# Optimization experiments

Measured on AMD Instinct MI355X. Metric: run time of the kernel, lower is better.

## Reference

```python
import jax, jax.numpy as jnp
import numpy as np

TEM = 0.5
BN_EPS = 1e-5
ROWS, IN_FEA, OUT_FEA = 16384, 512, 128


def setup_inputs() -> dict:
    key = jax.random.key(0)
    ks = jax.random.split(key, 3)
    doc_fea = jax.random.normal(ks[0], (ROWS, IN_FEA), dtype=jnp.float32)
    W1 = jax.random.normal(ks[1], (IN_FEA, OUT_FEA), dtype=jnp.float32) * 0.02
    b1 = jnp.zeros((OUT_FEA,), dtype=jnp.float32)
    gamma = jnp.ones((OUT_FEA,), dtype=jnp.float32)
    beta = jnp.zeros((OUT_FEA,), dtype=jnp.float32)
    W2 = jax.random.normal(ks[2], (OUT_FEA, OUT_FEA), dtype=jnp.float32) * 0.02
    b2 = jnp.zeros((OUT_FEA,), dtype=jnp.float32)
    return {"doc_fea": doc_fea, "W1": W1, "b1": b1, "gamma": gamma,
            "beta": beta, "W2": W2, "b2": b2}


def _l2_normalize(x):
    # matches torch F.normalize(dim=1, eps=1e-12)
    n = jnp.linalg.norm(x, axis=1, keepdims=True)
    return x / jnp.maximum(n, 1e-12)


def _half_loss(a, b):
    # rows of a, b are unit-norm, so cosine sim == matmul
    between = jnp.exp(a @ b.T / TEM)          # [N, N]
    refl = jnp.exp(a @ a.T / TEM)             # [N, N]
    pos = jnp.diagonal(between)
    denom = refl.sum(axis=1) + between.sum(axis=1) - jnp.diagonal(refl)
    return -jnp.log(pos / denom)


def reference(doc_fea, W1, b1, gamma, beta, W2, b2):
    # projector: Linear -> BatchNorm1d (training stats) -> ReLU -> Linear
    h = doc_fea @ W1 + b1
    mu = h.mean(axis=0)
    var = h.var(axis=0)  # biased variance, as used by torch BN normalization
    h = (h - mu) * jax.lax.rsqrt(var + BN_EPS) * gamma + beta
    h = jax.nn.relu(h)
    out = h @ W2 + b2
    out = _l2_normalize(out)
    # original: out_1 = out[indices where i%2!=0], out_2 = out[i%2==0]
    out_1 = out[1::2]
    out_2 = out[0::2]
    l1 = _half_loss(out_1, out_2)
    l2 = _half_loss(out_2, out_1)
    loss = (l1 + l2) * 0.5
    return loss.mean()
```

## Files before the change

kernel.cpp:

```cpp
#include <hip/hip_runtime.h>

typedef __attribute__((ext_vector_type(8))) short short8;
typedef __attribute__((ext_vector_type(4))) float f32x4;

typedef const __attribute__((address_space(1))) unsigned int as1_u32;
typedef __attribute__((address_space(3))) unsigned int as3_u32;

#define E2f   7.38905609893065f
#define OSCALE 1.69864357f

#define EXP2(x) exp2f(x)

__device__ inline unsigned short f2bf(float f){
    union { float f; unsigned int u; } x; x.f = f;
    unsigned int u = x.u;
    return (unsigned short)((u + 0x7fffu + ((u >> 16) & 1u)) >> 16);
}

__device__ inline short8 pack8(float4 a, float4 b){
    short8 t;
    t[0]=(short)f2bf(a.x); t[1]=(short)f2bf(a.y); t[2]=(short)f2bf(a.z); t[3]=(short)f2bf(a.w);
    t[4]=(short)f2bf(b.x); t[5]=(short)f2bf(b.y); t[6]=(short)f2bf(b.z); t[7]=(short)f2bf(b.w);
    return t;
}

__global__ __launch_bounds__(256) void k_prep(const float* __restrict__ W1, const float* __restrict__ W2,
                                              short* __restrict__ W1T, short* __restrict__ W2T){
    int idx = blockIdx.x*256 + threadIdx.x;
    if(idx < 512*128){
        int n = idx >> 9, k = idx & 511;
        W1T[idx] = (short)f2bf(W1[k*128 + n]);
    } else {
        int i2 = idx - 512*128;
        int n = i2 >> 7, k = i2 & 127;
        W2T[i2] = (short)f2bf(W2[k*128 + n]);
    }
}

__global__ __launch_bounds__(256) void k_gemm1(const float* __restrict__ doc, const float* __restrict__ b1,
                                               const short* __restrict__ W1T, float* __restrict__ h,
                                               float* __restrict__ bsum, float* __restrict__ bsq){
    int bid = blockIdx.x;
    int tid = threadIdx.x;
    int w = tid >> 6, l = tid & 63, lr = l & 15, lk = l >> 4;
    int rowA = bid*64 + w*16 + lr;

    short8 a[16];
    const float* dp = doc + rowA*512 + lk*8;
    #pragma unroll
    for(int c=0;c<16;c++){
        float4 f0 = *(const float4*)(dp + c*32);
        float4 f1 = *(const float4*)(dp + c*32 + 4);
        a[c] = pack8(f0, f1);
    }

    f32x4 acc[8];
    #pragma unroll
    for(int ct=0; ct<8; ct++) acc[ct] = (f32x4){0.f,0.f,0.f,0.f};

    const short* wb = W1T + lr*512 + lk*8;
    #pragma unroll
    for(int c=0;c<16;c++){
        #pragma unroll
        for(int ct=0; ct<8; ct++){
            short8 b = *(const short8*)(wb + ct*16*512 + c*32);
            acc[ct] = __builtin_amdgcn_mfma_f32_16x16x32_bf16(a[c], b, acc[ct], 0,0,0);
        }
    }

    __shared__ float lds_s[4][128];
    __shared__ float lds_q[4][128];
    int rowD = bid*64 + w*16 + lk*4;
    #pragma unroll
    for(int ct=0; ct<8; ct++){
        float bb = b1[ct*16 + lr];
        float s = 0.f, q = 0.f;
        #pragma unroll
        for(int r=0;r<4;r++){
            float v = acc[ct][r] + bb;
            h[(rowD + r)*128 + ct*16 + lr] = v;
            s += v; q += v*v;
        }
        s += __shfl_xor(s,16); s += __shfl_xor(s,32);
        q += __shfl_xor(q,16); q += __shfl_xor(q,32);
        if(lk==0){ lds_s[w][ct*16+lr] = s; lds_q[w][ct*16+lr] = q; }
    }
    __syncthreads();
    if(tid < 128){
        float S = lds_s[0][tid]+lds_s[1][tid]+lds_s[2][tid]+lds_s[3][tid];
        float Q = lds_q[0][tid]+lds_q[1][tid]+lds_q[2][tid]+lds_q[3][tid];
        bsum[bid*128 + tid] = S;
        bsq [bid*128 + tid] = Q;
    }
}

__global__ __launch_bounds__(1024) void k_bnfin(const float* __restrict__ bsum, const float* __restrict__ bsq,
                                                const float* __restrict__ gamma, const float* __restrict__ beta,
                                                float* __restrict__ bnA, float* __restrict__ bnB){
    int tid = threadIdx.x;
    int c = tid & 127, seg = tid >> 7;
    float S=0.f, Q=0.f;
    for(int b=seg*32; b<seg*32+32; b++){ S += bsum[b*128+c]; Q += bsq[b*128+c]; }
    __shared__ float ls[8][128], lq[8][128];
    ls[seg][c] = S; lq[seg][c] = Q;
    __syncthreads();
    if(tid < 128){
        float St=0.f, Qt=0.f;
        #pragma unroll
        for(int s=0;s<8;s++){ St += ls[s][tid]; Qt += lq[s][tid]; }
        float mu = St * (1.0f/16384.0f);
        float var = Qt * (1.0f/16384.0f) - mu*mu;
        float A = gamma[tid] * rsqrtf(var + 1e-5f);
        bnA[tid] = A;
        bnB[tid] = beta[tid] - mu*A;
    }
}

__global__ __launch_bounds__(256) void k_gemm2(const float* __restrict__ h, const short* __restrict__ W2T,
                                               const float* __restrict__ bnA, const float* __restrict__ bnB,
                                               const float* __restrict__ b2,
                                               short* __restrict__ o1s, short* __restrict__ o2s,
                                               float* __restrict__ dvec){
    int bid = blockIdx.x;
    int tid = threadIdx.x;
    int w = tid >> 6, l = tid & 63, lr = l & 15, lk = l >> 4;
    int rowA = bid*64 + w*16 + lr;

    short8 a[4];
    const float* hp = h + rowA*128 + lk*8;
    #pragma unroll
    for(int c=0;c<4;c++){
        float4 h0 = *(const float4*)(hp + c*32);
        float4 h1 = *(const float4*)(hp + c*32 + 4);
        float4 A0 = *(const float4*)(bnA + c*32 + lk*8);
        float4 A1 = *(const float4*)(bnA + c*32 + lk*8 + 4);
        float4 B0 = *(const float4*)(bnB + c*32 + lk*8);
        float4 B1 = *(const float4*)(bnB + c*32 + lk*8 + 4);
        float4 v0, v1;
        v0.x = fmaxf(h0.x*A0.x + B0.x, 0.f); v0.y = fmaxf(h0.y*A0.y + B0.y, 0.f);
        v0.z = fmaxf(h0.z*A0.z + B0.z, 0.f); v0.w = fmaxf(h0.w*A0.w + B0.w, 0.f);
        v1.x = fmaxf(h1.x*A1.x + B1.x, 0.f); v1.y = fmaxf(h1.y*A1.y + B1.y, 0.f);
        v1.z = fmaxf(h1.z*A1.z + B1.z, 0.f); v1.w = fmaxf(h1.w*A1.w + B1.w, 0.f);
        a[c] = pack8(v0, v1);
    }

    f32x4 acc[8];
    #pragma unroll
    for(int ct=0; ct<8; ct++) acc[ct] = (f32x4){0.f,0.f,0.f,0.f};
    const short* wb = W2T + lr*128 + lk*8;
    #pragma unroll
    for(int c=0;c<4;c++){
        #pragma unroll
        for(int ct=0; ct<8; ct++){
            short8 b = *(const short8*)(wb + ct*16*128 + c*32);
            acc[ct] = __builtin_amdgcn_mfma_f32_16x16x32_bf16(a[c], b, acc[ct], 0,0,0);
        }
    }

    #pragma unroll
    for(int ct=0; ct<8; ct++){
        float bb = b2[ct*16 + lr];
        #pragma unroll
        for(int r=0;r<4;r++) acc[ct][r] += bb;
    }
    float n2[4] = {0.f,0.f,0.f,0.f};
    #pragma unroll
    for(int ct=0; ct<8; ct++){
        #pragma unroll
        for(int r=0;r<4;r++) n2[r] += acc[ct][r]*acc[ct][r];
    }
    #pragma unroll
    for(int r=0;r<4;r++){
        n2[r] += __shfl_xor(n2[r],1); n2[r] += __shfl_xor(n2[r],2);
        n2[r] += __shfl_xor(n2[r],4); n2[r] += __shfl_xor(n2[r],8);
    }
    float sc[4];
    #pragma unroll
    for(int r=0;r<4;r++) sc[r] = 1.0f / fmaxf(sqrtf(n2[r]), 1e-12f);
    #pragma unroll
    for(int ct=0; ct<8; ct++){
        #pragma unroll
        for(int r=0;r<4;r++) acc[ct][r] *= sc[r];
    }
    float dp0 = 0.f, dp1 = 0.f;
    #pragma unroll
    for(int ct=0; ct<8; ct++){
        dp0 += acc[ct][0]*acc[ct][1];
        dp1 += acc[ct][2]*acc[ct][3];
    }
    dp0 += __shfl_xor(dp0,1); dp0 += __shfl_xor(dp0,2); dp0 += __shfl_xor(dp0,4); dp0 += __shfl_xor(dp0,8);
    dp1 += __shfl_xor(dp1,1); dp1 += __shfl_xor(dp1,2); dp1 += __shfl_xor(dp1,4); dp1 += __shfl_xor(dp1,8);
    int r0 = bid*64 + w*16 + lk*4;
    if(lr==0){
        dvec[(r0>>1)    ] = dp0;
        dvec[(r0>>1) + 1] = dp1;
    }
    #pragma unroll
    for(int ct=0; ct<8; ct++){
        #pragma unroll
        for(int r=0;r<4;r++){
            int grow = r0 + r;
            int col  = ct*16 + lr;
            short bits = (short)f2bf(acc[ct][r] * OSCALE);
            if(grow & 1) o1s[(grow>>1)*128 + col] = bits;
            else         o2s[(grow>>1)*128 + col] = bits;
        }
    }
}

__global__ __launch_bounds__(256) void k_sim(const short* __restrict__ o1s, const short* __restrict__ o2s,
                                             float* __restrict__ r11p, float* __restrict__ r22p,
                                             float* __restrict__ r12p, float* __restrict__ r21p){
    int bx = blockIdx.x, by = blockIdx.y, pz = blockIdx.z;
    const short* A = (pz & 1) ? o2s : o1s;
    const short* B = (pz==1 || pz==2) ? o2s : o1s;
    float* rowp = (pz==0) ? r11p : (pz==1 ? r22p : (pz==2 ? r12p : r21p));

    int tid = threadIdx.x;
    int w = tid>>6, l = tid&63, lr = l&15, lk = l>>4;

    __shared__ __align__(16) short lds[2][4096];

    short8 a[2][4];
    {
        const short* ap = A + (bx*128 + w*32 + lr)*128 + lk*8;
        #pragma unroll
        for(int rt=0;rt<2;rt++)
            #pragma unroll
            for(int c=0;c<4;c++)
                a[rt][c] = *(const short8*)(ap + rt*2048 + c*32);
    }

    int sb[4];
    #pragma unroll
    for(int c=0;c<4;c++) sb[c] = lr*256 + ((((c*4+lk) ^ (lr&7)))<<4);

    const short* gsrc[2];
    #pragma unroll
    for(int i=0;i<2;i++){
        int chunk = i*4 + w;
        int row = chunk*4 + (l>>4);
        int col16 = (l&15) ^ (row&7);
        gsrc[i] = B + (by*512 + row)*128 + col16*8;
    }

    #pragma unroll
    for(int i=0;i<2;i++){
        __builtin_amdgcn_global_load_lds((as1_u32*)gsrc[i],
            (as3_u32*)(&lds[0][(i*4+w)*512]), 16, 0, 0);
        gsrc[i] += 4096;
    }
    asm volatile("s_waitcnt vmcnt(0)" ::: "memory");
    __syncthreads();

    const f32x4 z4 = (f32x4){0.f,0.f,0.f,0.f};
    float rs[2][4] = {{0.f,0.f,0.f,0.f},{0.f,0.f,0.f,0.f}};
    int buf = 0;
    const char* lbase = (const char*)&lds[0][0];

    for(int t=0;t<16;t++){
        if(t<15){
            #pragma unroll
            for(int i=0;i<2;i++){
                __builtin_amdgcn_global_load_lds((as1_u32*)gsrc[i],
                    (as3_u32*)(&lds[buf^1][(i*4+w)*512]), 16, 0, 0);
                gsrc[i] += 4096;
            }
        }
        const char* lb = lbase + buf*8192;
        #pragma unroll
        for(int jt=0;jt<2;jt++){
            short8 b0 = *(const short8*)(lb + jt*4096 + sb[0]);
            short8 b1 = *(const short8*)(lb + jt*4096 + sb[1]);
            short8 b2 = *(const short8*)(lb + jt*4096 + sb[2]);
            short8 b3 = *(const short8*)(lb + jt*4096 + sb[3]);
            f32x4 c0, c1;
            c0 = __builtin_amdgcn_mfma_f32_16x16x32_bf16(a[0][0], b0, z4,0,0,0);
            c1 = __builtin_amdgcn_mfma_f32_16x16x32_bf16(a[1][0], b0, z4,0,0,0);
            c0 = __builtin_amdgcn_mfma_f32_16x16x32_bf16(a[0][1], b1, c0,0,0,0);
            c1 = __builtin_amdgcn_mfma_f32_16x16x32_bf16(a[1][1], b1, c1,0,0,0);
            c0 = __builtin_amdgcn_mfma_f32_16x16x32_bf16(a[0][2], b2, c0,0,0,0);
            c1 = __builtin_amdgcn_mfma_f32_16x16x32_bf16(a[1][2], b2, c1,0,0,0);
            c0 = __builtin_amdgcn_mfma_f32_16x16x32_bf16(a[0][3], b3, c0,0,0,0);
            c1 = __builtin_amdgcn_mfma_f32_16x16x32_bf16(a[1][3], b3, c1,0,0,0);
            rs[0][0] += EXP2(c0[0]); rs[0][1] += EXP2(c0[1]);
            rs[0][2] += EXP2(c0[2]); rs[0][3] += EXP2(c0[3]);
            rs[1][0] += EXP2(c1[0]); rs[1][1] += EXP2(c1[1]);
            rs[1][2] += EXP2(c1[2]); rs[1][3] += EXP2(c1[3]);
        }
        asm volatile("s_waitcnt vmcnt(0)" ::: "memory");
        __syncthreads();
        buf ^= 1;
    }

    #pragma unroll
    for(int rt=0;rt<2;rt++){
        #pragma unroll
        for(int r=0;r<4;r++){
            rs[rt][r] += __shfl_xor(rs[rt][r],1);
            rs[rt][r] += __shfl_xor(rs[rt][r],2);
            rs[rt][r] += __shfl_xor(rs[rt][r],4);
            rs[rt][r] += __shfl_xor(rs[rt][r],8);
        }
        if(lr==0){
            float4 v; v.x=rs[rt][0]; v.y=rs[rt][1]; v.z=rs[rt][2]; v.w=rs[rt][3];
            *(float4*)(rowp + by*8192 + bx*128 + w*32 + rt*16 + lk*4) = v;
        }
    }
}

__global__ __launch_bounds__(256) void k_loss1(const float* __restrict__ r11, const float* __restrict__ r22,
                                               const float* __restrict__ r12, const float* __restrict__ r21,
                                               const float* __restrict__ dvec, float* __restrict__ lpart){
    int i = blockIdx.x*256 + threadIdx.x;
    float s11=0.f, s22=0.f, s12=0.f, s21=0.f;
    #pragma unroll
    for(int s=0;s<16;s++){
        s11 += r11[s*8192+i]; s22 += r22[s*8192+i];
        s12 += r12[s*8192+i]; s21 += r21[s*8192+i];
    }
    float d1 = s11 - E2f + s12;
    float d2 = s22 - E2f + s21;
    float loss = 0.5f*(logf(d1)+logf(d2)) - 2.0f*dvec[i];
    loss += __shfl_xor(loss,1);  loss += __shfl_xor(loss,2);  loss += __shfl_xor(loss,4);
    loss += __shfl_xor(loss,8);  loss += __shfl_xor(loss,16); loss += __shfl_xor(loss,32);
    __shared__ float lds[4];
    if((threadIdx.x & 63) == 0) lds[threadIdx.x >> 6] = loss;
    __syncthreads();
    if(threadIdx.x == 0) lpart[blockIdx.x] = lds[0]+lds[1]+lds[2]+lds[3];
}

__global__ __launch_bounds__(64) void k_loss2(const float* __restrict__ lpart, float* __restrict__ out){
    if(threadIdx.x == 0){
        float s = 0.f;
        for(int i=0;i<32;i++) s += lpart[i];
        out[0] = s * (1.0f/8192.0f);
    }
}

extern "C" void kernel_launch(void* const* d_in, const int* in_sizes, int n_in,
                              void* d_out, int out_size, void* d_ws, size_t ws_size,
                              hipStream_t stream){
    (void)in_sizes; (void)n_in; (void)out_size; (void)ws_size;
    const float* doc   = (const float*)d_in[0];
    const float* W1    = (const float*)d_in[1];
    const float* b1    = (const float*)d_in[2];
    const float* gamma = (const float*)d_in[3];
    const float* beta  = (const float*)d_in[4];
    const float* W2    = (const float*)d_in[5];
    const float* b2    = (const float*)d_in[6];
    float* out = (float*)d_out;

    char* ws = (char*)d_ws;
    float* h     = (float*)(ws + 0);
    float* r11p  = (float*)(ws + 0);
    float* r22p  = (float*)(ws + 524288);
    float* r12p  = (float*)(ws + 1048576);
    float* r21p  = (float*)(ws + 1572864);
    short* W1T   = (short*)(ws + 8388608);
    short* W2T   = (short*)(ws + 8519680);
    short* o1s   = (short*)(ws + 8552448);
    short* o2s   = (short*)(ws + 10649600);
    float* dvec  = (float*)(ws + 12746752);
    float* bnA   = (float*)(ws + 12779520);
    float* bnB   = (float*)(ws + 12780032);
    float* bsum  = (float*)(ws + 12780544);
    float* bsq   = (float*)(ws + 12911616);
    float* lpart = (float*)(ws + 13042688);

    k_prep <<<320, 256, 0, stream>>>(W1, W2, W1T, W2T);
    k_gemm1<<<256, 256, 0, stream>>>(doc, b1, W1T, h, bsum, bsq);
    k_bnfin<<<1, 1024, 0, stream>>>(bsum, bsq, gamma, beta, bnA, bnB);
    k_gemm2<<<256, 256, 0, stream>>>(h, W2T, bnA, bnB, b2, o1s, o2s, dvec);
    dim3 sg(64, 16, 4);
    k_sim  <<<sg, 256, 0, stream>>>(o1s, o2s, r11p, r22p, r12p, r21p);
    k_loss1<<<32, 256, 0, stream>>>(r11p, r22p, r12p, r21p, dvec, lpart);
    k_loss2<<<1, 64, 0, stream>>>(lpart, out);
}
```

Measured before the change: 152.8 us.

## Triple-buffer similarity tile loads and use raw hardware exp2

```diff
diff --git a/kernel.cpp b/kernel.cpp
--- a/kernel.cpp
+++ b/kernel.cpp
@@ -9,7 +9,15 @@
 #define E2f   7.38905609893065f
 #define OSCALE 1.69864357f
 
-#define EXP2(x) exp2f(x)
+__device__ inline float fexp2(float x){
+#if __has_builtin(__builtin_amdgcn_exp2f)
+    return __builtin_amdgcn_exp2f(x);
+#else
+    float r;
+    asm("v_exp_f32 %0, %1" : "=v"(r) : "v"(x));
+    return r;
+#endif
+}
 
 __device__ inline unsigned short f2bf(float f){
     union { float f; unsigned int u; } x; x.f = f;
@@ -219,7 +227,7 @@
     int tid = threadIdx.x;
     int w = tid>>6, l = tid&63, lr = l&15, lk = l>>4;
 
-    __shared__ __align__(16) short lds[2][4096];
+    __shared__ __align__(16) short lds[3][4096];
 
     short8 a[2][4];
     {
@@ -245,29 +253,36 @@
     }
 
     #pragma unroll
-    for(int i=0;i<2;i++){
-        __builtin_amdgcn_global_load_lds((as1_u32*)gsrc[i],
-            (as3_u32*)(&lds[0][(i*4+w)*512]), 16, 0, 0);
-        gsrc[i] += 4096;
-    }
-    asm volatile("s_waitcnt vmcnt(0)" ::: "memory");
-    __syncthreads();
+    for(int b=0;b<2;b++){
+        #pragma unroll
+        for(int i=0;i<2;i++){
+            __builtin_amdgcn_global_load_lds((as1_u32*)gsrc[i],
+                (as3_u32*)(&lds[b][(i*4+w)*512]), 16, 0, 0);
+            gsrc[i] += 4096;
+        }
+    }
 
     const f32x4 z4 = (f32x4){0.f,0.f,0.f,0.f};
     float rs[2][4] = {{0.f,0.f,0.f,0.f},{0.f,0.f,0.f,0.f}};
-    int buf = 0;
     const char* lbase = (const char*)&lds[0][0];
 
     for(int t=0;t<16;t++){
-        if(t<15){
+        if(t < 15) asm volatile("s_waitcnt vmcnt(2)" ::: "memory");
+        else       asm volatile("s_waitcnt vmcnt(0)" ::: "memory");
+        __builtin_amdgcn_s_barrier();
+        __builtin_amdgcn_sched_barrier(0);
+
+        if(t+2 < 16){
+            char* dst = (char*)lbase + ((t+2)%3)*8192;
             #pragma unroll
             for(int i=0;i<2;i++){
                 __builtin_amdgcn_global_load_lds((as1_u32*)gsrc[i],
-                    (as3_u32*)(&lds[buf^1][(i*4+w)*512]), 16, 0, 0);
+                    (as3_u32*)(dst + (i*4+w)*1024), 16, 0, 0);
                 gsrc[i] += 4096;
             }
         }
-        const char* lb = lbase + buf*8192;
+
+        const char* lb = lbase + (t%3)*8192;
         #pragma unroll
         for(int jt=0;jt<2;jt++){
             short8 b0 = *(const short8*)(lb + jt*4096 + sb[0]);
@@ -283,14 +298,11 @@
             c1 = __builtin_amdgcn_mfma_f32_16x16x32_bf16(a[1][2], b2, c1,0,0,0);
             c0 = __builtin_amdgcn_mfma_f32_16x16x32_bf16(a[0][3], b3, c0,0,0,0);
             c1 = __builtin_amdgcn_mfma_f32_16x16x32_bf16(a[1][3], b3, c1,0,0,0);
-            rs[0][0] += EXP2(c0[0]); rs[0][1] += EXP2(c0[1]);
-            rs[0][2] += EXP2(c0[2]); rs[0][3] += EXP2(c0[3]);
-            rs[1][0] += EXP2(c1[0]); rs[1][1] += EXP2(c1[1]);
-            rs[1][2] += EXP2(c1[2]); rs[1][3] += EXP2(c1[3]);
-        }
-        asm volatile("s_waitcnt vmcnt(0)" ::: "memory");
-        __syncthreads();
-        buf ^= 1;
+            rs[0][0] += fexp2(c0[0]); rs[0][1] += fexp2(c0[1]);
+            rs[0][2] += fexp2(c0[2]); rs[0][3] += fexp2(c0[3]);
+            rs[1][0] += fexp2(c1[0]); rs[1][1] += fexp2(c1[1]);
+            rs[1][2] += fexp2(c1[2]); rs[1][3] += fexp2(c1[3]);
+        }
     }
 
     #pragma unroll
```

Result: faster. 143.4 us (-6.2%).
